# Kernel tuning notes

Hardware: AMD Instinct MI355X
Metric: run time of the kernel (lower is better)

## Reference

```python
import jax, jax.numpy as jnp
import numpy as np

VOCAB = 50000
TAGSET = 10
NUM_TAGS = TAGSET - 1
EMB = 256
HID = 512          # BiLSTM hidden_dim; each direction uses HID // 2
B, S = 64, 256


def setup_inputs() -> dict:
    key = jax.random.key(0)
    ks = jax.random.split(key, 20)
    Hd = HID // 2
    sc = 0.1
    emb_table = jax.random.normal(ks[0], (VOCAB, EMB), jnp.float32) * sc
    emb_table = emb_table.at[0].set(0.0)  # padding_idx=0
    inp = {
        "inputs": jax.random.randint(ks[1], (B, S), 1, VOCAB),
        "tags": jax.random.randint(ks[2], (B, S), 1, TAGSET),
        "mask": jnp.ones((B, S), jnp.bool_),
        "emb_table": emb_table,
        "w_ih_f": jax.random.normal(ks[3], (4 * Hd, EMB), jnp.float32) * sc,
        "w_hh_f": jax.random.normal(ks[4], (4 * Hd, Hd), jnp.float32) * sc,
        "b_ih_f": jax.random.normal(ks[5], (4 * Hd,), jnp.float32) * sc,
        "b_hh_f": jax.random.normal(ks[6], (4 * Hd,), jnp.float32) * sc,
        "w_ih_b": jax.random.normal(ks[7], (4 * Hd, EMB), jnp.float32) * sc,
        "w_hh_b": jax.random.normal(ks[8], (4 * Hd, Hd), jnp.float32) * sc,
        "b_ih_b": jax.random.normal(ks[9], (4 * Hd,), jnp.float32) * sc,
        "b_hh_b": jax.random.normal(ks[10], (4 * Hd,), jnp.float32) * sc,
        "w_out": jax.random.normal(ks[11], (TAGSET, HID), jnp.float32) * sc,
        "b_out": jax.random.normal(ks[12], (TAGSET,), jnp.float32) * sc,
        "start_trans": jax.random.normal(ks[13], (NUM_TAGS,), jnp.float32) * sc,
        "end_trans": jax.random.normal(ks[14], (NUM_TAGS,), jnp.float32) * sc,
        "trans": jax.random.normal(ks[15], (NUM_TAGS, NUM_TAGS), jnp.float32) * sc,
    }
    return inp


def _run_lstm(xs, w_ih, w_hh, b):
    # xs: (S, B, E) -> hs: (S, B, Hd); torch gate order i, f, g, o
    Hd = w_hh.shape[1]
    h0 = jnp.zeros((xs.shape[1], Hd), xs.dtype)

    def step(carry, x_t):
        h, c = carry
        z = x_t @ w_ih.T + h @ w_hh.T + b
        i, f, g, o = jnp.split(z, 4, axis=-1)
        c = jax.nn.sigmoid(f) * c + jax.nn.sigmoid(i) * jnp.tanh(g)
        h = jax.nn.sigmoid(o) * jnp.tanh(c)
        return (h, c), h

    _, hs = jax.lax.scan(step, (h0, h0), xs)
    return hs


def _crf_loss(emissions, tags_s, mask_s, start_trans, end_trans, trans):
    # emissions: (S, B, T); tags_s, mask_s: (S, B)
    nb = emissions.shape[1]
    ar = jnp.arange(nb)
    maskf = mask_s.astype(emissions.dtype)

    # numerator: score of the gold path
    num0 = start_trans[tags_s[0]] + emissions[0, ar, tags_s[0]]

    def num_step(carry, inp):
        score, prev = carry
        em_t, tag_t, m_t = inp
        score = score + (trans[prev, tag_t] + em_t[ar, tag_t]) * m_t
        prev = jnp.where(m_t > 0, tag_t, prev)  # track last valid tag
        return (score, prev), None

    (num, last_tags), _ = jax.lax.scan(
        num_step, (num0, tags_s[0]), (emissions[1:], tags_s[1:], maskf[1:]))
    num = num + end_trans[last_tags]

    # denominator: forward algorithm (logsumexp recurrence)
    def den_step(score, inp):
        em_t, m_t = inp
        nxt = jax.nn.logsumexp(
            score[:, :, None] + trans[None] + em_t[:, None, :], axis=1)
        return jnp.where(m_t[:, None], nxt, score), None

    score0 = start_trans[None] + emissions[0]
    score, _ = jax.lax.scan(den_step, score0, (emissions[1:], mask_s[1:]))
    den = jax.nn.logsumexp(score + end_trans[None], axis=1)

    return -(num - den).mean()


def reference(inputs, tags, mask, emb_table, w_ih_f, w_hh_f, b_ih_f, b_hh_f,
              w_ih_b, w_hh_b, b_ih_b, b_hh_b, w_out, b_out,
              start_trans, end_trans, trans):
    emb = emb_table[inputs]                 # (B, S, E)
    xs = emb.transpose(1, 0, 2)             # (S, B, E)
    h_f = _run_lstm(xs, w_ih_f, w_hh_f, b_ih_f + b_hh_f)
    h_b = _run_lstm(xs[::-1], w_ih_b, w_hh_b, b_ih_b + b_hh_b)[::-1]
    h = jnp.concatenate([h_f, h_b], axis=-1)  # (S, B, HID); dropout = identity (eval)
    emissions = h @ w_out.T + b_out           # (S, B, TAGSET)
    emissions = emissions[:, :, 1:]           # drop pad tag column
    tags_s = (tags - 1).T                      # (S, B), shifted to CRF tag space
    mask_s = mask.T                            # (S, B)
    return _crf_loss(emissions, tags_s, mask_s, start_trans, end_trans, trans)
```

## Files before the change

kernel.cpp:

```cpp
#include <hip/hip_runtime.h>
#include <hip/hip_bf16.h>
#include <stdint.h>

#define S_LEN 256
#define BATCH 64
#define HD 256
#define NT 9
#define NTOK (S_LEN*BATCH)

typedef _Float16 hf2 __attribute__((ext_vector_type(2)));
typedef short bf16x8 __attribute__((ext_vector_type(8)));
typedef float f32x4 __attribute__((ext_vector_type(4)));

__device__ __forceinline__ float sigf(float x){ return 1.f/(1.f+__expf(-x)); }
__device__ __forceinline__ float tanh_(float x){ return 1.f - 2.f/(__expf(2.f*x)+1.f); }
__device__ __forceinline__ float wredsum(float v){
#pragma unroll
  for (int s = 32; s > 0; s >>= 1) v += __shfl_xor(v, s);
  return v;
}
__device__ __forceinline__ uint16_t f2b(float f){
  __hip_bfloat16 h = __float2bfloat16(f);
  return *(uint16_t*)&h;
}
__device__ __forceinline__ float b2f(uint16_t u){
  union{uint32_t i; float f;} a; a.i = ((uint32_t)u)<<16; return a.f;
}

__device__ __forceinline__ int sdot4(uint32_t a, uint32_t b, int c){
#if __has_builtin(__builtin_amdgcn_sdot4)
  return __builtin_amdgcn_sdot4((int)a, (int)b, c, false);
#else
  int r = c;
#pragma unroll
  for (int e = 0; e < 4; ++e) {
    int av = (int)(signed char)((a >> (8*e)) & 0xff);
    int bv = (int)(signed char)((b >> (8*e)) & 0xff);
    r += av * bv;
  }
  return r;
#endif
}

__device__ __forceinline__ int qadd_xor1(int v){
#if __has_builtin(__builtin_amdgcn_update_dpp)
  return v + __builtin_amdgcn_update_dpp(0, v, 0xB1, 0xF, 0xF, false);
#else
  return v + __shfl_xor(v, 1);
#endif
}
__device__ __forceinline__ int qadd_xor2(int v){
#if __has_builtin(__builtin_amdgcn_update_dpp)
  return v + __builtin_amdgcn_update_dpp(0, v, 0x4E, 0xF, 0xF, false);
#else
  return v + __shfl_xor(v, 2);
#endif
}

__device__ __forceinline__ int rotrow4(int v){
#if __has_builtin(__builtin_amdgcn_update_dpp)
  int a = __builtin_amdgcn_update_dpp(0, v, 0x114, 0xF, 0xF, true);
  int b = __builtin_amdgcn_update_dpp(0, v, 0x10C, 0xF, 0xF, true);
  return a | b;
#else
  int l = (int)(threadIdx.x & 63);
  return __shfl(v, (l & 48) | ((l + 4) & 15), 64);
#endif
}
__device__ __forceinline__ uint4 rotrow4x4(uint4 v){
  uint4 r;
  r.x = (uint32_t)rotrow4((int)v.x);
  r.y = (uint32_t)rotrow4((int)v.y);
  r.z = (uint32_t)rotrow4((int)v.z);
  r.w = (uint32_t)rotrow4((int)v.w);
  return r;
}

__global__ __launch_bounds__(256) void prep_all(const int* __restrict__ inp,
    const float* __restrict__ emb,
    const float* __restrict__ wihf, const float* __restrict__ wihb,
    const float* __restrict__ bif, const float* __restrict__ bhf,
    const float* __restrict__ bib, const float* __restrict__ bhb,
    const float* __restrict__ whf, const float* __restrict__ whb,
    uint16_t* __restrict__ wih16, float* __restrict__ bias,
    uint16_t* __restrict__ gemb, float* __restrict__ mult){
  int blk = blockIdx.x, t = threadIdx.x;
  int idx = blk*256 + t;
  {
    int n = idx >> 8, k = idx & 255;
    const float* w = (n < 1024) ? wihf : wihb;
    wih16[idx] = f2b(w[(n & 1023)*256 + k]);
    if (idx < 2048)
      bias[idx] = (idx < 1024) ? (bif[idx] + bhf[idx]) : (bib[idx-1024] + bhb[idx-1024]);
  }
  {
    int m = idx >> 5;
    int k8 = (idx & 31)*8;
    int tok = inp[(m & 63)*S_LEN + (m >> 6)];
    const float* src = emb + (size_t)tok*256 + k8;
    float4 v0 = *(const float4*)(src);
    float4 v1 = *(const float4*)(src+4);
    uint16_t t16[8];
    t16[0]=f2b(v0.x); t16[1]=f2b(v0.y); t16[2]=f2b(v0.z); t16[3]=f2b(v0.w);
    t16[4]=f2b(v1.x); t16[5]=f2b(v1.y); t16[6]=f2b(v1.z); t16[7]=f2b(v1.w);
    *(uint4*)&gemb[(size_t)m*256 + k8] = *(uint4*)t16;
  }
  if (t < 64) {
    int dir = blk >> 10, col = blk & 1023;
    const float* w = (dir ? whb : whf) + (size_t)col*256 + t*4;
    float4 v = *(const float4*)w;
    float amax = fmaxf(fmaxf(fabsf(v.x), fabsf(v.y)), fmaxf(fabsf(v.z), fabsf(v.w)));
#pragma unroll
    for (int s = 32; s > 0; s >>= 1) amax = fmaxf(amax, __shfl_xor(amax, s));
    if (t == 0) mult[blk] = amax / 16129.f;
  }
}

__global__ void prep_pack10(const float* __restrict__ whf, const float* __restrict__ whb,
                            const float* __restrict__ mult, uint32_t* __restrict__ wpk){
  int idx = blockIdx.x*256 + threadIdx.x;
  int s = idx >> 17;
  int rem = idx & 131071;
  int dir = rem >> 16;
  int rem2 = rem & 65535;
  int r = rem2 >> 10;
  int tid = rem2 & 1023;
  int g = r >> 4, p = r & 15;
  int d = p >> 2, e = p & 3;
  int j = tid >> 2, ks = tid & 3;
  int q0 = j & 3;
  int q = s ? ((q0 - d) & 3) : ((q0 + d) & 3);
  int col = g*256 + j;
  const float* w = (dir ? whb : whf) + (size_t)col*256 + ks*64 + q*16 + e*4;
  float sw = mult[dir*1024 + col] * 127.f;
  float inv = (sw > 0.f) ? (1.f/sw) : 0.f;
  uint32_t pk = 0;
#pragma unroll
  for (int el = 0; el < 4; ++el) {
    float qv = rintf(w[el] * inv);
    qv = fminf(127.f, fmaxf(-127.f, qv));
    int qi = (int)qv;
    pk |= ((uint32_t)(qi & 0xff)) << (8*el);
  }
  wpk[idx] = pk;
}

__global__ __launch_bounds__(256, 2) void inproj_mfma3(const uint16_t* __restrict__ gemb,
    const uint16_t* __restrict__ wih16, const float* __restrict__ bias,
    uint16_t* __restrict__ xgf, uint16_t* __restrict__ xgb){
  __shared__ uint16_t As[128][72];
  __shared__ uint16_t Bs[128][72];
  int flat = blockIdx.x + blockIdx.y*16;
  int nf = (flat & 7)*256 + (flat >> 3);
  int bn = nf & 15, bm = nf >> 4;
  int tid = threadIdx.x;
  int w = tid >> 6, l = tid & 63;
  int lr = l & 15, lg = l >> 4;
  f32x4 acc[2][8];
#pragma unroll
  for (int am = 0; am < 2; ++am)
#pragma unroll
    for (int cf = 0; cf < 8; ++cf) acc[am][cf] = (f32x4){0.f,0.f,0.f,0.f};

  int sr = tid >> 1, sh = tid & 1;

  for (int k0 = 0; k0 < 256; k0 += 64) {
    {
      const uint16_t* asrc = gemb + (size_t)(bm*128 + sr)*256 + k0 + sh*32;
      uint4 a0 = *(const uint4*)(asrc+0);
      uint4 a1 = *(const uint4*)(asrc+8);
      uint4 a2 = *(const uint4*)(asrc+16);
      uint4 a3 = *(const uint4*)(asrc+24);
      *(uint4*)&As[sr][sh*32+0]  = a0;
      *(uint4*)&As[sr][sh*32+8]  = a1;
      *(uint4*)&As[sr][sh*32+16] = a2;
      *(uint4*)&As[sr][sh*32+24] = a3;
    }
    {
      const uint16_t* bsrc = wih16 + (size_t)(bn*128 + sr)*256 + k0 + sh*32;
      uint4 b0 = *(const uint4*)(bsrc+0);
      uint4 b1 = *(const uint4*)(bsrc+8);
      uint4 b2 = *(const uint4*)(bsrc+16);
      uint4 b3 = *(const uint4*)(bsrc+24);
      *(uint4*)&Bs[sr][sh*32+0]  = b0;
      *(uint4*)&Bs[sr][sh*32+8]  = b1;
      *(uint4*)&Bs[sr][sh*32+16] = b2;
      *(uint4*)&Bs[sr][sh*32+24] = b3;
    }
    __syncthreads();
#pragma unroll
    for (int ks = 0; ks < 2; ++ks) {
      int koff = ks*32 + lg*8;
      bf16x8 a0 = *(const bf16x8*)&As[32*w + lr][koff];
      bf16x8 a1 = *(const bf16x8*)&As[32*w + 16 + lr][koff];
#pragma unroll
      for (int cf = 0; cf < 8; ++cf) {
        bf16x8 b = *(const bf16x8*)&Bs[cf*16 + lr][koff];
        acc[0][cf] = __builtin_amdgcn_mfma_f32_16x16x32_bf16(a0, b, acc[0][cf], 0, 0, 0);
        acc[1][cf] = __builtin_amdgcn_mfma_f32_16x16x32_bf16(a1, b, acc[1][cf], 0, 0, 0);
      }
    }
    __syncthreads();
  }
  int n0 = bn*128;
  bool back = (n0 >= 1024);
  uint16_t* dst = back ? xgb : xgf;
  int nb0 = back ? (n0 - 1024) : n0;
#pragma unroll
  for (int cf = 0; cf < 8; ++cf) {
    int nc = cf*16 + lr;
    int nd = nb0 + nc;
    int gj = (nd & 255)*4 + (nd >> 8);
    float bv = bias[n0 + nc];
#pragma unroll
    for (int am = 0; am < 2; ++am)
#pragma unroll
    for (int r = 0; r < 4; ++r) {
      int m = bm*128 + 32*w + am*16 + lg*4 + r;
      dst[(size_t)m*1024 + gj] = f2b(acc[am][cf][r] + bv);
    }
  }
}

__global__ __launch_bounds__(1024, 4)
void lstm12(const uint32_t* __restrict__ wpk, const float* __restrict__ mult,
    const uint16_t* __restrict__ xgf, const uint16_t* __restrict__ xgb,
    __hip_bfloat16* __restrict__ hout){
  int dir = blockIdx.x >> 6;
  int b = blockIdx.x & 63;
  int tid = threadIdx.x;
  int j = tid >> 2, ks = tid & 3;
  int q0 = j & 3;
  __shared__ __align__(16) uint32_t hs8[2][64];

#if __has_builtin(__builtin_amdgcn_update_dpp)
  int lane = tid & 63;
  int u = __builtin_amdgcn_update_dpp(0, lane, 0x114, 0xF, 0xF, true);
  int probe = __builtin_amdgcn_readlane(u, 4);
  int sel = (probe == 0) ? 1 : 0;
#else
  int sel = 0;
#endif

  const uint32_t* wp = wpk + (size_t)sel*131072 + (size_t)dir*65536 + tid;
  uint32_t wreg[64];
#pragma unroll
  for (int r = 0; r < 64; ++r) wreg[r] = wp[(size_t)r*1024];
#pragma unroll
  for (int r = 0; r < 64; ++r) asm volatile("" : "+v"(wreg[r]));
  asm volatile("" ::: "memory");

  float m4[4];
#pragma unroll
  for (int g = 0; g < 4; ++g) m4[g] = mult[dir*1024 + g*256 + j];

  if (tid < 128) hs8[tid >> 6][tid & 63] = 0u;
  float cst = 0.f;
  const uint16_t* xgp = (dir ? xgb : xgf) + (size_t)b*1024 + j*4;
  __syncthreads();

  int ts0 = dir ? (S_LEN-1) : 0;
  int ts1 = dir ? (S_LEN-2) : 1;
  uint2 xA = *(const uint2*)(xgp + (size_t)ts0*65536);
  uint2 xB = *(const uint2*)(xgp + (size_t)ts1*65536);
  for (int t = 0; t < S_LEN; ++t) {
    int ts = dir ? (S_LEN-1-t) : t;
    int cur = t & 1;
    uint2 xC = xB;
    if (t + 2 < S_LEN) {
      int tn = dir ? (S_LEN-3-t) : (t+2);
      xC = *(const uint2*)(xgp + (size_t)tn*65536);
    }
    uint4 hq0 = *(const uint4*)&hs8[cur][ks*16 + q0*4];
    uint4 hq1 = rotrow4x4(hq0);
    uint4 hq2 = rotrow4x4(hq1);
    uint4 hq3 = rotrow4x4(hq2);
    int zi[4] = {0,0,0,0};
#pragma unroll
    for (int g = 0; g < 4; ++g) {
      const uint32_t* wg_ = &wreg[g*16];
      zi[g] = sdot4(wg_[0],  hq0.x, zi[g]);
      zi[g] = sdot4(wg_[1],  hq0.y, zi[g]);
      zi[g] = sdot4(wg_[2],  hq0.z, zi[g]);
      zi[g] = sdot4(wg_[3],  hq0.w, zi[g]);
      zi[g] = sdot4(wg_[4],  hq1.x, zi[g]);
      zi[g] = sdot4(wg_[5],  hq1.y, zi[g]);
      zi[g] = sdot4(wg_[6],  hq1.z, zi[g]);
      zi[g] = sdot4(wg_[7],  hq1.w, zi[g]);
      zi[g] = sdot4(wg_[8],  hq2.x, zi[g]);
      zi[g] = sdot4(wg_[9],  hq2.y, zi[g]);
      zi[g] = sdot4(wg_[10], hq2.z, zi[g]);
      zi[g] = sdot4(wg_[11], hq2.w, zi[g]);
      zi[g] = sdot4(wg_[12], hq3.x, zi[g]);
      zi[g] = sdot4(wg_[13], hq3.y, zi[g]);
      zi[g] = sdot4(wg_[14], hq3.z, zi[g]);
      zi[g] = sdot4(wg_[15], hq3.w, zi[g]);
    }
#pragma unroll
    for (int g = 0; g < 4; ++g) zi[g] = qadd_xor1(zi[g]);
#pragma unroll
    for (int g = 0; g < 4; ++g) zi[g] = qadd_xor2(zi[g]);
    float zf[4];
    zf[0] = (float)zi[0]*m4[0] + b2f((uint16_t)(xA.x & 0xffff));
    zf[1] = (float)zi[1]*m4[1] + b2f((uint16_t)(xA.x >> 16));
    zf[2] = (float)zi[2]*m4[2] + b2f((uint16_t)(xA.y & 0xffff));
    zf[3] = (float)zi[3]*m4[3] + b2f((uint16_t)(xA.y >> 16));
    float ig = sigf(zf[0]), fg = sigf(zf[1]), gg = tanh_(zf[2]), og = sigf(zf[3]);
    cst = fg*cst + ig*gg;
    float hj = og * tanh_(cst);
    if (ks == 0) {
      int q = (int)rintf(hj * 127.f);
      ((unsigned char*)&hs8[cur^1][0])[j] = (unsigned char)(q & 0xff);
      hout[((size_t)ts*BATCH + b)*512 + dir*256 + j] = __float2bfloat16(hj);
    }
    __builtin_amdgcn_sched_barrier(0);
    asm volatile("s_waitcnt lgkmcnt(0)" ::: "memory");
    __builtin_amdgcn_sched_barrier(0);
    __builtin_amdgcn_s_barrier();
    __builtin_amdgcn_sched_barrier(0);
    xA = xB; xB = xC;
  }
}

__global__ __launch_bounds__(256) void outproj2(const __hip_bfloat16* __restrict__ hb,
    const float* __restrict__ w_out, const float* __restrict__ b_out,
    float* __restrict__ em){
  __shared__ float wsm[NT*512];
  __shared__ float bsm[NT];
  int tid = threadIdx.x;
  for (int i = tid; i < NT*512; i += 256) wsm[i] = w_out[512 + i];
  if (tid < NT) bsm[tid] = b_out[1 + tid];
  __syncthreads();
  int wave = tid >> 6, l = tid & 63;
#pragma unroll
  for (int it = 0; it < 4; ++it) {
    int m = blockIdx.x*16 + it*4 + wave;
    const __hip_bfloat16* hp = hb + (size_t)m*512;
    float hv[8];
#pragma unroll
    for (int q = 0; q < 8; ++q) hv[q] = __bfloat162float(hp[l + 64*q]);
    for (int jj = 0; jj < NT; ++jj) {
      float p = 0.f;
#pragma unroll
      for (int q = 0; q < 8; ++q) p += hv[q]*wsm[jj*512 + 64*q + l];
      p = wredsum(p);
      if (l == 0) em[(size_t)m*NT + jj] = p + bsm[jj];
    }
  }
}

__global__ __launch_bounds__(64) void crf(const int* __restrict__ tags,
    const float* __restrict__ em, const float* __restrict__ start_t,
    const float* __restrict__ end_t, const float* __restrict__ trans,
    float* __restrict__ part){
  int b = blockIdx.x;
  int l = threadIdx.x;
  float np = 0.f;
  for (int t = l; t < S_LEN; t += 64) {
    int tg = tags[b*S_LEN + t] - 1;
    float e = em[(size_t)(t*BATCH + b)*NT + tg];
    float tr = (t == 0) ? start_t[tg] : trans[(tags[b*S_LEN + t - 1] - 1)*NT + tg];
    np += e + tr;
  }
  float num = wredsum(np);
  num += end_t[tags[b*S_LEN + S_LEN-1] - 1];
  int j = (l < NT) ? l : 0;
  float tj[NT];
#pragma unroll
  for (int i = 0; i < NT; ++i) tj[i] = trans[i*NT + j];
  float sc = start_t[j] + em[(size_t)b*NT + j];
  for (int t = 1; t < S_LEN; ++t) {
    float e = em[(size_t)(t*BATCH + b)*NT + j];
    float m = -1e30f;
    float vals[NT];
#pragma unroll
    for (int i = 0; i < NT; ++i) { float si = __shfl(sc, i); vals[i] = si + tj[i]; m = fmaxf(m, vals[i]); }
    float ssum = 0.f;
#pragma unroll
    for (int i = 0; i < NT; ++i) ssum += __expf(vals[i] - m);
    sc = e + m + __logf(ssum);
  }
  float vj = (l < NT) ? (sc + end_t[l]) : -1e30f;
  float mx = vj;
#pragma unroll
  for (int s2 = 32; s2 > 0; s2 >>= 1) mx = fmaxf(mx, __shfl_xor(mx, s2));
  float es = __expf(vj - mx);
  es = wredsum(es);
  if (l == 0) part[b] = num - (mx + __logf(es));
}

__global__ void finalize(const float* __restrict__ part, float* __restrict__ out){
  float v = part[threadIdx.x];
  v = wredsum(v);
  if (threadIdx.x == 0) out[0] = -(v / 64.f);
}

extern "C" void kernel_launch(void* const* d_in, const int* in_sizes, int n_in,
                              void* d_out, int out_size, void* d_ws, size_t ws_size,
                              hipStream_t stream) {
  (void)in_sizes; (void)n_in; (void)out_size; (void)ws_size;
  const int*   inputs  = (const int*)d_in[0];
  const int*   tags    = (const int*)d_in[1];
  const float* emb     = (const float*)d_in[3];
  const float* w_ih_f  = (const float*)d_in[4];
  const float* w_hh_f  = (const float*)d_in[5];
  const float* b_ih_f  = (const float*)d_in[6];
  const float* b_hh_f  = (const float*)d_in[7];
  const float* w_ih_b  = (const float*)d_in[8];
  const float* w_hh_b  = (const float*)d_in[9];
  const float* b_ih_b  = (const float*)d_in[10];
  const float* b_hh_b  = (const float*)d_in[11];
  const float* w_out   = (const float*)d_in[12];
  const float* b_out   = (const float*)d_in[13];
  const float* start_t = (const float*)d_in[14];
  const float* end_t   = (const float*)d_in[15];
  const float* trans   = (const float*)d_in[16];

  char* ws = (char*)d_ws;
  size_t off = 0;
  auto alloc = [&](size_t bytes) -> void* {
    void* p = ws + off;
    off = (off + bytes + 255) & ~(size_t)255;
    return p;
  };
  uint16_t* xgf = (uint16_t*)alloc((size_t)NTOK*1024*2);
  uint16_t* xgb = (uint16_t*)alloc((size_t)NTOK*1024*2);
  __hip_bfloat16* hbf = (__hip_bfloat16*)alloc((size_t)NTOK*512*2);
  float*    em    = (float*)alloc((size_t)NTOK*NT*4);
  uint16_t* wih16 = (uint16_t*)alloc((size_t)2048*256*2);
  uint16_t* gemb  = (uint16_t*)alloc((size_t)NTOK*256*2);
  float*    bias  = (float*)alloc((size_t)2048*4);
  float*    mult  = (float*)alloc((size_t)2048*4);
  uint32_t* wpk   = (uint32_t*)alloc((size_t)2*2*64*1024*4);
  float*    part  = (float*)alloc((size_t)64*4);

  prep_all<<<2048, 256, 0, stream>>>(inputs, emb, w_ih_f, w_ih_b, b_ih_f, b_hh_f,
                                     b_ih_b, b_hh_b, w_hh_f, w_hh_b,
                                     wih16, bias, gemb, mult);
  prep_pack10<<<1024, 256, 0, stream>>>(w_hh_f, w_hh_b, mult, wpk);
  inproj_mfma3<<<dim3(16, 128), 256, 0, stream>>>(gemb, wih16, bias, xgf, xgb);
  lstm12<<<128, 1024, 0, stream>>>(wpk, mult, xgf, xgb, hbf);
  outproj2<<<1024, 256, 0, stream>>>(hbf, w_out, b_out, em);
  crf<<<64, 64, 0, stream>>>(tags, em, start_t, end_t, trans, part);
  finalize<<<1, 64, 0, stream>>>(part, (float*)d_out);
}
```

Measured before the change: 532.1 us.

## Run LSTM recurrence with int8 MFMA over 16-batch tiles in 8 workgroups

Replaces the per-batch-element sdot4 recurrence (128 workgroups, one per direction and batch element) with an MFMA-based recurrence. Each of 8 workgroups handles 16 batch elements for one direction and computes the hidden-to-gate product with v_mfma_i32_16x16x64_i8, with weights repacked into MFMA fragment layout held in registers. This trades many small workgroups doing dot-product chains for fewer workgroups using matrix cores. It also drops the xg prefetch pipelining, bakes the MFMA output latency into fixed s_nop padding, and leaves most CUs idle during the serial scan.

```diff
diff --git a/kernel.cpp b/kernel.cpp
--- a/kernel.cpp
+++ b/kernel.cpp
@@ -11,6 +11,8 @@
 typedef _Float16 hf2 __attribute__((ext_vector_type(2)));
 typedef short bf16x8 __attribute__((ext_vector_type(8)));
 typedef float f32x4 __attribute__((ext_vector_type(4)));
+typedef int i32x4 __attribute__((ext_vector_type(4)));
+typedef uint32_t u32x4 __attribute__((ext_vector_type(4)));
 
 __device__ __forceinline__ float sigf(float x){ return 1.f/(1.f+__expf(-x)); }
 __device__ __forceinline__ float tanh_(float x){ return 1.f - 2.f/(__expf(2.f*x)+1.f); }
@@ -25,55 +27,6 @@
 }
 __device__ __forceinline__ float b2f(uint16_t u){
   union{uint32_t i; float f;} a; a.i = ((uint32_t)u)<<16; return a.f;
-}
-
-__device__ __forceinline__ int sdot4(uint32_t a, uint32_t b, int c){
-#if __has_builtin(__builtin_amdgcn_sdot4)
-  return __builtin_amdgcn_sdot4((int)a, (int)b, c, false);
-#else
-  int r = c;
-#pragma unroll
-  for (int e = 0; e < 4; ++e) {
-    int av = (int)(signed char)((a >> (8*e)) & 0xff);
-    int bv = (int)(signed char)((b >> (8*e)) & 0xff);
-    r += av * bv;
-  }
-  return r;
-#endif
-}
-
-__device__ __forceinline__ int qadd_xor1(int v){
-#if __has_builtin(__builtin_amdgcn_update_dpp)
-  return v + __builtin_amdgcn_update_dpp(0, v, 0xB1, 0xF, 0xF, false);
-#else
-  return v + __shfl_xor(v, 1);
-#endif
-}
-__device__ __forceinline__ int qadd_xor2(int v){
-#if __has_builtin(__builtin_amdgcn_update_dpp)
-  return v + __builtin_amdgcn_update_dpp(0, v, 0x4E, 0xF, 0xF, false);
-#else
-  return v + __shfl_xor(v, 2);
-#endif
-}
-
-__device__ __forceinline__ int rotrow4(int v){
-#if __has_builtin(__builtin_amdgcn_update_dpp)
-  int a = __builtin_amdgcn_update_dpp(0, v, 0x114, 0xF, 0xF, true);
-  int b = __builtin_amdgcn_update_dpp(0, v, 0x10C, 0xF, 0xF, true);
-  return a | b;
-#else
-  int l = (int)(threadIdx.x & 63);
-  return __shfl(v, (l & 48) | ((l + 4) & 15), 64);
-#endif
-}
-__device__ __forceinline__ uint4 rotrow4x4(uint4 v){
-  uint4 r;
-  r.x = (uint32_t)rotrow4((int)v.x);
-  r.y = (uint32_t)rotrow4((int)v.y);
-  r.z = (uint32_t)rotrow4((int)v.z);
-  r.w = (uint32_t)rotrow4((int)v.w);
-  return r;
 }
 
 __global__ __launch_bounds__(256) void prep_all(const int* __restrict__ inp,
@@ -116,31 +69,29 @@
   }
 }
 
-__global__ void prep_pack10(const float* __restrict__ whf, const float* __restrict__ whb,
+__global__ void prep_pack11(const float* __restrict__ whf, const float* __restrict__ whb,
                             const float* __restrict__ mult, uint32_t* __restrict__ wpk){
   int idx = blockIdx.x*256 + threadIdx.x;
-  int s = idx >> 17;
-  int rem = idx & 131071;
-  int dir = rem >> 16;
-  int rem2 = rem & 65535;
-  int r = rem2 >> 10;
-  int tid = rem2 & 1023;
-  int g = r >> 4, p = r & 15;
-  int d = p >> 2, e = p & 3;
-  int j = tid >> 2, ks = tid & 3;
-  int q0 = j & 3;
-  int q = s ? ((q0 - d) & 3) : ((q0 + d) & 3);
-  int col = g*256 + j;
-  const float* w = (dir ? whb : whf) + (size_t)col*256 + ks*64 + q*16 + e*4;
+  int d = idx & 3;
+  int r = (idx >> 2) & 15;
+  int tid = (idx >> 6) & 1023;
+  int dir = idx >> 16;
+  int w = tid >> 6, l = tid & 63;
+  int nt = r >> 2, kc = r & 3;
+  int n = w*64 + nt*16 + (l & 15);
+  int gate = n & 3, unit = n >> 2;
+  int col = gate*256 + unit;
+  int kbase = kc*64 + (l >> 4)*16 + d*4;
+  const float* wsrc = (dir ? whb : whf) + (size_t)col*256 + kbase;
   float sw = mult[dir*1024 + col] * 127.f;
   float inv = (sw > 0.f) ? (1.f/sw) : 0.f;
   uint32_t pk = 0;
 #pragma unroll
-  for (int el = 0; el < 4; ++el) {
-    float qv = rintf(w[el] * inv);
-    qv = fminf(127.f, fmaxf(-127.f, qv));
-    int qi = (int)qv;
-    pk |= ((uint32_t)(qi & 0xff)) << (8*el);
+  for (int e = 0; e < 4; ++e) {
+    float q = rintf(wsrc[e] * inv);
+    q = fminf(127.f, fmaxf(-127.f, q));
+    int qi = (int)q;
+    pk |= ((uint32_t)(qi & 0xff)) << (8*e);
   }
   wpk[idx] = pk;
 }
@@ -216,109 +167,95 @@
     for (int am = 0; am < 2; ++am)
 #pragma unroll
     for (int r = 0; r < 4; ++r) {
-      int m = bm*128 + 32*w + am*16 + lg*4 + r;
-      dst[(size_t)m*1024 + gj] = f2b(acc[am][cf][r] + bv);
+      int mix = bm*128 + 32*w + am*16 + lg*4 + r;
+      dst[(size_t)mix*1024 + gj] = f2b(acc[am][cf][r] + bv);
     }
   }
 }
 
 __global__ __launch_bounds__(1024, 4)
-void lstm12(const uint32_t* __restrict__ wpk, const float* __restrict__ mult,
+void lstm13(const uint32_t* __restrict__ wpk, const float* __restrict__ mult,
     const uint16_t* __restrict__ xgf, const uint16_t* __restrict__ xgb,
     __hip_bfloat16* __restrict__ hout){
-  int dir = blockIdx.x >> 6;
-  int b = blockIdx.x & 63;
+  int wg = blockIdx.x;
+  int dir = wg >> 2;
+  int cb = (wg & 3) * 16;
   int tid = threadIdx.x;
-  int j = tid >> 2, ks = tid & 3;
-  int q0 = j & 3;
-  __shared__ __align__(16) uint32_t hs8[2][64];
-
-#if __has_builtin(__builtin_amdgcn_update_dpp)
-  int lane = tid & 63;
-  int u = __builtin_amdgcn_update_dpp(0, lane, 0x114, 0xF, 0xF, true);
-  int probe = __builtin_amdgcn_readlane(u, 4);
-  int sel = (probe == 0) ? 1 : 0;
-#else
-  int sel = 0;
-#endif
-
-  const uint32_t* wp = wpk + (size_t)sel*131072 + (size_t)dir*65536 + tid;
-  uint32_t wreg[64];
-#pragma unroll
-  for (int r = 0; r < 64; ++r) wreg[r] = wp[(size_t)r*1024];
-#pragma unroll
-  for (int r = 0; r < 64; ++r) asm volatile("" : "+v"(wreg[r]));
+  int l = tid & 63, w = tid >> 6;
+  int m = l & 15, rg = l >> 4;
+  __shared__ __align__(16) unsigned char hsb[8192];
+
+  const u32x4* wp4 = (const u32x4*)wpk + (size_t)(dir*1024 + tid)*16;
+  u32x4 wfrag[16];
+#pragma unroll
+  for (int r = 0; r < 16; ++r) wfrag[r] = wp4[r];
+#pragma unroll
+  for (int r = 0; r < 16; ++r) asm volatile("" : "+v"(wfrag[r]));
   asm volatile("" ::: "memory");
 
-  float m4[4];
-#pragma unroll
-  for (int g = 0; g < 4; ++g) m4[g] = mult[dir*1024 + g*256 + j];
-
-  if (tid < 128) hs8[tid >> 6][tid & 63] = 0u;
-  float cst = 0.f;
-  const uint16_t* xgp = (dir ? xgb : xgf) + (size_t)b*1024 + j*4;
+  int unitv[4];
+  uint32_t mmlo[4], mmhi[4];
+#pragma unroll
+  for (int nt = 0; nt < 4; ++nt) {
+    int unit = w*16 + nt*4 + rg;
+    unitv[nt] = unit;
+    const float* mp = mult + dir*1024 + unit;
+    mmlo[nt] = (uint32_t)f2b(mp[0])   | ((uint32_t)f2b(mp[256]) << 16);
+    mmhi[nt] = (uint32_t)f2b(mp[512]) | ((uint32_t)f2b(mp[768]) << 16);
+  }
+
+  uint32_t* hs32 = (uint32_t*)hsb;
+  hs32[tid] = 0u;
+  hs32[tid + 1024] = 0u;
+  float cst[4] = {0.f, 0.f, 0.f, 0.f};
+  const uint16_t* xbase = (dir ? xgb : xgf) + (size_t)(cb + m)*1024;
   __syncthreads();
 
-  int ts0 = dir ? (S_LEN-1) : 0;
-  int ts1 = dir ? (S_LEN-2) : 1;
-  uint2 xA = *(const uint2*)(xgp + (size_t)ts0*65536);
-  uint2 xB = *(const uint2*)(xgp + (size_t)ts1*65536);
   for (int t = 0; t < S_LEN; ++t) {
     int ts = dir ? (S_LEN-1-t) : t;
     int cur = t & 1;
-    uint2 xC = xB;
-    if (t + 2 < S_LEN) {
-      int tn = dir ? (S_LEN-3-t) : (t+2);
-      xC = *(const uint2*)(xgp + (size_t)tn*65536);
-    }
-    uint4 hq0 = *(const uint4*)&hs8[cur][ks*16 + q0*4];
-    uint4 hq1 = rotrow4x4(hq0);
-    uint4 hq2 = rotrow4x4(hq1);
-    uint4 hq3 = rotrow4x4(hq2);
-    int zi[4] = {0,0,0,0};
-#pragma unroll
-    for (int g = 0; g < 4; ++g) {
-      const uint32_t* wg_ = &wreg[g*16];
-      zi[g] = sdot4(wg_[0],  hq0.x, zi[g]);
-      zi[g] = sdot4(wg_[1],  hq0.y, zi[g]);
-      zi[g] = sdot4(wg_[2],  hq0.z, zi[g]);
-      zi[g] = sdot4(wg_[3],  hq0.w, zi[g]);
-      zi[g] = sdot4(wg_[4],  hq1.x, zi[g]);
-      zi[g] = sdot4(wg_[5],  hq1.y, zi[g]);
-      zi[g] = sdot4(wg_[6],  hq1.z, zi[g]);
-      zi[g] = sdot4(wg_[7],  hq1.w, zi[g]);
-      zi[g] = sdot4(wg_[8],  hq2.x, zi[g]);
-      zi[g] = sdot4(wg_[9],  hq2.y, zi[g]);
-      zi[g] = sdot4(wg_[10], hq2.z, zi[g]);
-      zi[g] = sdot4(wg_[11], hq2.w, zi[g]);
-      zi[g] = sdot4(wg_[12], hq3.x, zi[g]);
-      zi[g] = sdot4(wg_[13], hq3.y, zi[g]);
-      zi[g] = sdot4(wg_[14], hq3.z, zi[g]);
-      zi[g] = sdot4(wg_[15], hq3.w, zi[g]);
-    }
-#pragma unroll
-    for (int g = 0; g < 4; ++g) zi[g] = qadd_xor1(zi[g]);
-#pragma unroll
-    for (int g = 0; g < 4; ++g) zi[g] = qadd_xor2(zi[g]);
-    float zf[4];
-    zf[0] = (float)zi[0]*m4[0] + b2f((uint16_t)(xA.x & 0xffff));
-    zf[1] = (float)zi[1]*m4[1] + b2f((uint16_t)(xA.x >> 16));
-    zf[2] = (float)zi[2]*m4[2] + b2f((uint16_t)(xA.y & 0xffff));
-    zf[3] = (float)zi[3]*m4[3] + b2f((uint16_t)(xA.y >> 16));
-    float ig = sigf(zf[0]), fg = sigf(zf[1]), gg = tanh_(zf[2]), og = sigf(zf[3]);
-    cst = fg*cst + ig*gg;
-    float hj = og * tanh_(cst);
-    if (ks == 0) {
-      int q = (int)rintf(hj * 127.f);
-      ((unsigned char*)&hs8[cur^1][0])[j] = (unsigned char)(q & 0xff);
-      hout[((size_t)ts*BATCH + b)*512 + dir*256 + j] = __float2bfloat16(hj);
+    const uint16_t* xp = xbase + (size_t)ts*65536;
+    uint2 xq[4];
+#pragma unroll
+    for (int nt = 0; nt < 4; ++nt) xq[nt] = *(const uint2*)(xp + unitv[nt]*4);
+
+    i32x4 acc[4];
+#pragma unroll
+    for (int nt = 0; nt < 4; ++nt) acc[nt] = (i32x4){0,0,0,0};
+    const unsigned char* rb = hsb + cur*4096;
+#pragma unroll
+    for (int kc = 0; kc < 4; ++kc) {
+      u32x4 bq = *(const u32x4*)(rb + (kc*4 + rg)*256 + m*16);
+#pragma unroll
+      for (int nt = 0; nt < 4; ++nt) {
+        asm volatile("v_mfma_i32_16x16x64_i8 %0, %1, %2, %0"
+                     : "+v"(acc[nt]) : "v"(wfrag[nt*4 + kc]), "v"(bq));
+      }
+    }
+    asm volatile("s_nop 7\n\ts_nop 7" ::: );
+    unsigned char* wb = hsb + (cur^1)*4096;
+#pragma unroll
+    for (int nt = 0; nt < 4; ++nt) {
+      float mg0 = b2f((uint16_t)(mmlo[nt] & 0xffff));
+      float mg1 = b2f((uint16_t)(mmlo[nt] >> 16));
+      float mg2 = b2f((uint16_t)(mmhi[nt] & 0xffff));
+      float mg3 = b2f((uint16_t)(mmhi[nt] >> 16));
+      float zi = (float)acc[nt][0]*mg0 + b2f((uint16_t)(xq[nt].x & 0xffff));
+      float zf = (float)acc[nt][1]*mg1 + b2f((uint16_t)(xq[nt].x >> 16));
+      float zg = (float)acc[nt][2]*mg2 + b2f((uint16_t)(xq[nt].y & 0xffff));
+      float zo = (float)acc[nt][3]*mg3 + b2f((uint16_t)(xq[nt].y >> 16));
+      float ig = sigf(zi), fg = sigf(zf), gg = tanh_(zg), og = sigf(zo);
+      cst[nt] = fg*cst[nt] + ig*gg;
+      float h = og * tanh_(cst[nt]);
+      int q = (int)rintf(h * 127.f);
+      wb[w*256 + m*16 + nt*4 + rg] = (unsigned char)(q & 0xff);
+      hout[((size_t)ts*BATCH + cb + m)*512 + dir*256 + unitv[nt]] = __float2bfloat16(h);
     }
     __builtin_amdgcn_sched_barrier(0);
     asm volatile("s_waitcnt lgkmcnt(0)" ::: "memory");
     __builtin_amdgcn_sched_barrier(0);
     __builtin_amdgcn_s_barrier();
     __builtin_amdgcn_sched_barrier(0);
-    xA = xB; xB = xC;
   }
 }
 
@@ -431,15 +368,15 @@
   uint16_t* gemb  = (uint16_t*)alloc((size_t)NTOK*256*2);
   float*    bias  = (float*)alloc((size_t)2048*4);
   float*    mult  = (float*)alloc((size_t)2048*4);
-  uint32_t* wpk   = (uint32_t*)alloc((size_t)2*2*64*1024*4);
+  uint32_t* wpk   = (uint32_t*)alloc((size_t)2*65536*4);
   float*    part  = (float*)alloc((size_t)64*4);
 
   prep_all<<<2048, 256, 0, stream>>>(inputs, emb, w_ih_f, w_ih_b, b_ih_f, b_hh_f,
                                      b_ih_b, b_hh_b, w_hh_f, w_hh_b,
                                      wih16, bias, gemb, mult);
-  prep_pack10<<<1024, 256, 0, stream>>>(w_hh_f, w_hh_b, mult, wpk);
+  prep_pack11<<<512, 256, 0, stream>>>(w_hh_f, w_hh_b, mult, wpk);
   inproj_mfma3<<<dim3(16, 128), 256, 0, stream>>>(gemb, wih16, bias, xgf, xgb);
-  lstm12<<<128, 1024, 0, stream>>>(wpk, mult, xgf, xgb, hbf);
+  lstm13<<<8, 1024, 0, stream>>>(wpk, mult, xgf, xgb, hbf);
   outproj2<<<1024, 256, 0, stream>>>(hbf, w_out, b_out, em);
   crf<<<64, 64, 0, stream>>>(tags, em, start_t, end_t, trans, part);
   finalize<<<1, 64, 0, stream>>>(part, (float*)d_out);
```

New measurement: 1.189 ms. +123.5%, slower.
